# Kernel optimization log

Hardware: AMD Instinct MI355X
Metric: run time of the kernel (lower is better)

## Reference

```python
import jax, jax.numpy as jnp
import numpy as np

DIM = 512
HEADS = 8
D_HEAD = 64
INNER = HEADS * D_HEAD  # 512
CTX_DIM = 768
FF_INNER = 4 * DIM  # 2048
SCALE = D_HEAD ** -0.5
LN_EPS = 1e-5


def layer_norm(x, g, b):
    mu = jnp.mean(x, axis=-1, keepdims=True)
    var = jnp.var(x, axis=-1, keepdims=True)
    return (x - mu) * jax.lax.rsqrt(var + LN_EPS) * g + b


def attention(x, ctx, qw, kw, vw, ow, ob):
    B, N, _ = x.shape
    M = ctx.shape[1]
    q = (x @ qw).reshape(B, N, HEADS, D_HEAD).transpose(0, 2, 1, 3)
    k = (ctx @ kw).reshape(B, M, HEADS, D_HEAD).transpose(0, 2, 1, 3)
    v = (ctx @ vw).reshape(B, M, HEADS, D_HEAD).transpose(0, 2, 1, 3)
    sim = jnp.einsum('bhid,bhjd->bhij', q, k) * SCALE  # [B,H,N,M]
    attn = jax.nn.softmax(sim, axis=-1)
    out = jnp.einsum('bhij,bhjd->bhid', attn, v)
    out = out.transpose(0, 2, 1, 3).reshape(B, N, INNER)
    return out @ ow + ob


def setup_inputs() -> dict:
    key = jax.random.key(0)
    ks = jax.random.split(key, 20)
    r = lambda k, shp, s=0.02: jax.random.normal(k, shp, dtype=jnp.float32) * s
    return {
        'x': jax.random.normal(ks[0], (2, 4096, DIM), dtype=jnp.float32),
        'context': jax.random.normal(ks[1], (2, 256, CTX_DIM), dtype=jnp.float32),
        'q1_w': r(ks[2], (DIM, INNER)), 'k1_w': r(ks[3], (DIM, INNER)),
        'v1_w': r(ks[4], (DIM, INNER)), 'o1_w': r(ks[5], (INNER, DIM)),
        'o1_b': jnp.zeros((DIM,), jnp.float32),
        'q2_w': r(ks[6], (DIM, INNER)), 'k2_w': r(ks[7], (CTX_DIM, INNER)),
        'v2_w': r(ks[8], (CTX_DIM, INNER)), 'o2_w': r(ks[9], (INNER, DIM)),
        'o2_b': jnp.zeros((DIM,), jnp.float32),
        'ff_in_w': r(ks[10], (DIM, 2 * FF_INNER)), 'ff_in_b': jnp.zeros((2 * FF_INNER,), jnp.float32),
        'ff_out_w': r(ks[11], (FF_INNER, DIM)), 'ff_out_b': jnp.zeros((DIM,), jnp.float32),
        'ln1_g': jnp.ones((DIM,), jnp.float32), 'ln1_b': jnp.zeros((DIM,), jnp.float32),
        'ln2_g': jnp.ones((DIM,), jnp.float32), 'ln2_b': jnp.zeros((DIM,), jnp.float32),
        'ln3_g': jnp.ones((DIM,), jnp.float32), 'ln3_b': jnp.zeros((DIM,), jnp.float32),
    }


def reference(x, context, q1_w, k1_w, v1_w, o1_w, o1_b,
              q2_w, k2_w, v2_w, o2_w, o2_b,
              ff_in_w, ff_in_b, ff_out_w, ff_out_b,
              ln1_g, ln1_b, ln2_g, ln2_b, ln3_g, ln3_b):
    # self-attention + residual
    h = layer_norm(x, ln1_g, ln1_b)
    x = attention(h, h, q1_w, k1_w, v1_w, o1_w, o1_b) + x
    # cross-attention + residual
    h = layer_norm(x, ln2_g, ln2_b)
    x = attention(h, context, q2_w, k2_w, v2_w, o2_w, o2_b) + x
    # GEGLU feed-forward + residual (torch F.gelu is exact erf form)
    h = layer_norm(x, ln3_g, ln3_b)
    proj = h @ ff_in_w + ff_in_b
    val, gate = jnp.split(proj, 2, axis=-1)
    ff = (val * jax.nn.gelu(gate, approximate=False)) @ ff_out_w + ff_out_b
    return ff + x
```

## Files before the change

kernel.cpp:

```cpp
#include <hip/hip_runtime.h>
#include <hip/hip_bf16.h>
#include <cstdint>


typedef __bf16 bf16_t;
typedef __bf16 bf16x8 __attribute__((ext_vector_type(8)));
typedef float f32x4 __attribute__((ext_vector_type(4)));
typedef float f32x16 __attribute__((ext_vector_type(16)));

__device__ __forceinline__ bf16_t f2bf(float f) { return (bf16_t)f; }

__device__ __forceinline__ f32x4 mfma16(bf16x8 a, bf16x8 b, f32x4 c) {
  return __builtin_amdgcn_mfma_f32_16x16x32_bf16(a, b, c, 0, 0, 0);
}
__device__ __forceinline__ f32x16 mfma32(bf16x8 a, bf16x8 b, f32x16 c) {
  return __builtin_amdgcn_mfma_f32_32x32x16_bf16(a, b, c, 0, 0, 0);
}

__device__ __forceinline__ float gelu_exact(float x) {
  return 0.5f * x * (1.0f + erff(x * 0.70710678118654752f));
}

__device__ __forceinline__ void gload_lds16(const bf16_t* g, bf16_t* lds) {
  __builtin_amdgcn_global_load_lds(
      (const __attribute__((address_space(1))) unsigned int*)g,
      (__attribute__((address_space(3))) unsigned int*)lds, 16, 0, 0);
}

template <typename T>
__global__ __launch_bounds__(256) void ln_kernel(const T* __restrict__ in,
                                                 const float* __restrict__ gw,
                                                 const float* __restrict__ bw,
                                                 bf16_t* __restrict__ out) {
  int w = threadIdx.x >> 6, l = threadIdx.x & 63;
  size_t row = (size_t)blockIdx.x * 4 + w;
  float xs[8];
  if constexpr (sizeof(T) == 4) {
    const float* p = (const float*)in + row * 512 + l * 8;
    f32x4 va = *(const f32x4*)p;
    f32x4 vb = *(const f32x4*)(p + 4);
#pragma unroll
    for (int j = 0; j < 4; j++) { xs[j] = va[j]; xs[4 + j] = vb[j]; }
  } else {
    const bf16_t* p = (const bf16_t*)in + row * 512 + l * 8;
    bf16x8 v = *(const bf16x8*)p;
#pragma unroll
    for (int j = 0; j < 8; j++) xs[j] = (float)v[j];
  }
  float s = 0.f;
#pragma unroll
  for (int j = 0; j < 8; j++) s += xs[j];
#pragma unroll
  for (int m = 1; m < 64; m <<= 1) s += __shfl_xor(s, m);
  float mu = s * (1.0f / 512.0f);
  float v = 0.f;
#pragma unroll
  for (int j = 0; j < 8; j++) { float d = xs[j] - mu; v += d * d; }
#pragma unroll
  for (int m = 1; m < 64; m <<= 1) v += __shfl_xor(v, m);
  float rstd = rsqrtf(v * (1.0f / 512.0f) + 1e-5f);
  f32x4 g0 = *(const f32x4*)(gw + l * 8);
  f32x4 g1 = *(const f32x4*)(gw + l * 8 + 4);
  f32x4 b0 = *(const f32x4*)(bw + l * 8);
  f32x4 b1 = *(const f32x4*)(bw + l * 8 + 4);
  bf16x8 o;
#pragma unroll
  for (int j = 0; j < 4; j++) o[j] = f2bf((xs[j] - mu) * rstd * g0[j] + b0[j]);
#pragma unroll
  for (int j = 0; j < 4; j++) o[4 + j] = f2bf((xs[4 + j] - mu) * rstd * g1[j] + b1[j]);
  *(bf16x8*)(out + row * 512 + l * 8) = o;
}

struct WJob {
  const float* W;
  bf16_t* Wt;
  int K;
  int N;
  float sc;
  int tile0;
};
struct WJobs {
  WJob j[10];
};

__global__ __launch_bounds__(256) void wtrans_all_kernel(WJobs jobs) {
  __shared__ float t[32][33];
  int bid = blockIdx.x;
  int i = 0;
#pragma unroll
  for (int q = 1; q < 10; q++)
    if (bid >= jobs.j[q].tile0) i = q;
  WJob jb = jobs.j[i];
  int tt = bid - jb.tile0;
  int ktiles = jb.K >> 5;
  int k0 = (tt % ktiles) * 32, n0 = (tt / ktiles) * 32;
#pragma unroll
  for (int s = 0; s < 4; s++) {
    int idx = threadIdx.x + s * 256;
    int kk = idx >> 5, nn = idx & 31;
    t[kk][nn] = jb.W[(size_t)(k0 + kk) * jb.N + n0 + nn];
  }
  __syncthreads();
#pragma unroll
  for (int s = 0; s < 4; s++) {
    int idx = threadIdx.x + s * 256;
    int nn = idx >> 5, kk = idx & 31;
    jb.Wt[(size_t)(n0 + nn) * jb.K + k0 + kk] = f2bf(t[kk][nn] * jb.sc);
  }
}

__global__ __launch_bounds__(256) void cvt_kernel(const float* __restrict__ in,
                                                  bf16_t* __restrict__ out) {
  int i = (blockIdx.x * 256 + threadIdx.x) * 4;
  f32x4 v = *(const f32x4*)(in + i);
  out[i + 0] = f2bf(v[0]);
  out[i + 1] = f2bf(v[1]);
  out[i + 2] = f2bf(v[2]);
  out[i + 3] = f2bf(v[3]);
}

template <int BM, int BN, int EPI>
__global__ __launch_bounds__(256) void gemm_kernel(
    const bf16_t* __restrict__ A, const bf16_t* __restrict__ Bt,
    const float* __restrict__ bias, const void* __restrict__ res,
    void* __restrict__ outp, int M, int N, int K, int gateOff, int ldo) {
  constexpr int WR = BM / 2;
  constexpr int WN = BN / 2;
  constexpr int MF = WR / 16;
  constexpr int NF = WN / 16;
  constexpr int ABLK = BM / 64;
  constexpr int BROWS = (EPI == 2) ? 2 * BN : BN;
  constexpr int BBLK = BROWS / 64;
  __shared__ bf16_t Al[2][2][BM][32];
  __shared__ bf16_t Bl[2][2][BROWS][32];

  int tid = threadIdx.x;
  int w = tid >> 6, l = tid & 63;
  int wr = w >> 1, wc = w & 1;
  int lg = l >> 4, lc = l & 15;

  int ntiles = gridDim.y;
  int lin = blockIdx.y * gridDim.x + blockIdx.x;
  int cpx = (gridDim.x * gridDim.y) >> 3;
  int v = (lin & 7) * cpx + (lin >> 3);
  int m0 = (v / ntiles) * BM, n0 = (v % ntiles) * BN;

  f32x4 acc[MF][NF] = {};
  f32x4 acc2[MF][NF] = {};

  int srow = tid >> 2, scol = (tid & 3) * 8;
  const bf16_t* aP[ABLK];
#pragma unroll
  for (int i = 0; i < ABLK; i++)
    aP[i] = A + (size_t)(m0 + i * 64 + srow) * K + scol;
  const bf16_t* bP[BBLK];
  if (EPI == 2) {
    bP[0] = Bt + (size_t)(n0 + srow) * K + scol;
    bP[1] = Bt + (size_t)(n0 + gateOff + srow) * K + scol;
  } else {
#pragma unroll
    for (int i = 0; i < BBLK; i++)
      bP[i] = Bt + (size_t)(n0 + i * 64 + srow) * K + scol;
  }

  auto STAGE = [&](int buf, int k0) {
#pragma unroll
    for (int kh = 0; kh < 2; kh++) {
#pragma unroll
      for (int i = 0; i < ABLK; i++)
        gload_lds16(aP[i] + k0 + kh * 32, &Al[buf][kh][i * 64 + w * 16][0]);
#pragma unroll
      for (int i = 0; i < BBLK; i++)
        gload_lds16(bP[i] + k0 + kh * 32, &Bl[buf][kh][i * 64 + w * 16][0]);
    }
  };

  int nk = K / 64;
  int cur = 0;
  STAGE(0, 0);
  __syncthreads();

  for (int t = 0; t < nk; ++t) {
    if (t + 1 < nk) STAGE(cur ^ 1, (t + 1) * 64);

#pragma unroll
    for (int kh = 0; kh < 2; kh++) {
      bf16x8 af[MF];
#pragma unroll
      for (int mi = 0; mi < MF; mi++)
        af[mi] = *(const bf16x8*)&Al[cur][kh][wr * WR + mi * 16 + lc][lg * 8];
      bf16x8 bfr[NF];
#pragma unroll
      for (int ni = 0; ni < NF; ni++)
        bfr[ni] = *(const bf16x8*)&Bl[cur][kh][wc * WN + ni * 16 + lc][lg * 8];
#pragma unroll
      for (int mi = 0; mi < MF; mi++)
#pragma unroll
        for (int ni = 0; ni < NF; ni++)
          acc[mi][ni] = mfma16(af[mi], bfr[ni], acc[mi][ni]);
      if (EPI == 2) {
        bf16x8 bg[NF];
#pragma unroll
        for (int ni = 0; ni < NF; ni++)
          bg[ni] =
              *(const bf16x8*)&Bl[cur][kh][BN + wc * WN + ni * 16 + lc][lg * 8];
#pragma unroll
        for (int mi = 0; mi < MF; mi++)
#pragma unroll
          for (int ni = 0; ni < NF; ni++)
            acc2[mi][ni] = mfma16(af[mi], bg[ni], acc2[mi][ni]);
      }
    }
    __syncthreads();
    cur ^= 1;
  }

#pragma unroll
  for (int mi = 0; mi < MF; mi++) {
#pragma unroll
    for (int ni = 0; ni < NF; ni++) {
#pragma unroll
      for (int r = 0; r < 4; r++) {
        int row = m0 + wr * WR + mi * 16 + lg * 4 + r;
        int col = n0 + wc * WN + ni * 16 + lc;
        size_t idx = (size_t)row * ldo + col;
        float v2 = acc[mi][ni][r];
        if (EPI == 0) {
          ((bf16_t*)outp)[idx] = f2bf(v2);
        } else if (EPI == 3) {
          int cs = (col & ~15) | (lc & 3) | ((lc & 4) << 1) | ((lc & 8) >> 1);
          ((bf16_t*)outp)[(size_t)row * ldo + cs] = f2bf(v2);
        } else if (EPI == 4) {
          ((bf16_t*)outp)[idx] =
              f2bf(v2 + bias[col] + ((const float*)res)[idx]);
        } else if (EPI == 5) {
          ((bf16_t*)outp)[idx] =
              f2bf(v2 + bias[col] + (float)((const bf16_t*)res)[idx]);
        } else if (EPI == 6) {
          ((float*)outp)[idx] =
              v2 + bias[col] + (float)((const bf16_t*)res)[idx];
        } else {
          float g = acc2[mi][ni][r] + bias[col + gateOff];
          float val = v2 + bias[col];
          ((bf16_t*)outp)[idx] = f2bf(val * gelu_exact(g));
        }
      }
    }
  }
}

__global__ __launch_bounds__(256) void cross_fused_kernel(
    const bf16_t* __restrict__ hb, const bf16_t* __restrict__ q2t,
    bf16_t* __restrict__ qkb, const bf16_t* __restrict__ ctxb,
    const bf16_t* __restrict__ k2t, bf16_t* __restrict__ kb,
    const bf16_t* __restrict__ v2t, bf16_t* __restrict__ vtg2) {
  constexpr int BM = 64, BN = 128;
  constexpr int WR = 32, WN = 64, MF = 2, NF = 4;
  __shared__ bf16_t Al[2][2][BM][32];
  __shared__ bf16_t Bl[2][2][BN][32];

  const bf16_t* A;
  const bf16_t* Bt;
  bf16_t* outp;
  int K, m0;
  bool perm = false;
  if (blockIdx.z == 0) {
    A = hb; Bt = q2t; outp = qkb; K = 512; m0 = blockIdx.x * BM;
  } else {
    int bx = blockIdx.x;
    if (bx >= 16) return;
    K = 768;
    if (bx < 8) {
      A = ctxb; Bt = k2t; outp = kb; m0 = bx * BM;
    } else {
      A = v2t; Bt = ctxb; outp = vtg2; perm = true; m0 = (bx - 8) * BM;
    }
  }
  const int ldo = 512;
  int n0 = blockIdx.y * BN;

  int tid = threadIdx.x;
  int w = tid >> 6, l = tid & 63;
  int wr = w >> 1, wc = w & 1;
  int lg = l >> 4, lc = l & 15;

  f32x4 acc[MF][NF] = {};

  int srow = tid >> 2, scol = (tid & 3) * 8;
  const bf16_t* aP0 = A + (size_t)(m0 + srow) * K + scol;
  const bf16_t* bP0 = Bt + (size_t)(n0 + srow) * K + scol;
  const bf16_t* bP1 = Bt + (size_t)(n0 + 64 + srow) * K + scol;

  auto STAGE = [&](int buf, int k0) {
#pragma unroll
    for (int kh = 0; kh < 2; kh++) {
      gload_lds16(aP0 + k0 + kh * 32, &Al[buf][kh][w * 16][0]);
      gload_lds16(bP0 + k0 + kh * 32, &Bl[buf][kh][w * 16][0]);
      gload_lds16(bP1 + k0 + kh * 32, &Bl[buf][kh][64 + w * 16][0]);
    }
  };

  int nk = K / 64;
  int cur = 0;
  STAGE(0, 0);
  __syncthreads();

  for (int t = 0; t < nk; ++t) {
    if (t + 1 < nk) STAGE(cur ^ 1, (t + 1) * 64);
#pragma unroll
    for (int kh = 0; kh < 2; kh++) {
      bf16x8 af[MF];
#pragma unroll
      for (int mi = 0; mi < MF; mi++)
        af[mi] = *(const bf16x8*)&Al[cur][kh][wr * WR + mi * 16 + lc][lg * 8];
      bf16x8 bfr[NF];
#pragma unroll
      for (int ni = 0; ni < NF; ni++)
        bfr[ni] = *(const bf16x8*)&Bl[cur][kh][wc * WN + ni * 16 + lc][lg * 8];
#pragma unroll
      for (int mi = 0; mi < MF; mi++)
#pragma unroll
        for (int ni = 0; ni < NF; ni++)
          acc[mi][ni] = mfma16(af[mi], bfr[ni], acc[mi][ni]);
    }
    __syncthreads();
    cur ^= 1;
  }

#pragma unroll
  for (int mi = 0; mi < MF; mi++) {
#pragma unroll
    for (int ni = 0; ni < NF; ni++) {
#pragma unroll
      for (int r = 0; r < 4; r++) {
        int row = m0 + wr * WR + mi * 16 + lg * 4 + r;
        int col = n0 + wc * WN + ni * 16 + lc;
        int cs = perm ? ((col & ~15) | (lc & 3) | ((lc & 4) << 1) |
                         ((lc & 8) >> 1))
                      : col;
        outp[(size_t)row * ldo + cs] = f2bf(acc[mi][ni][r]);
      }
    }
  }
}

__global__ __launch_bounds__(256) void attn_kernel(
    const bf16_t* __restrict__ Q, int ldq, const bf16_t* __restrict__ Kb,
    int ldk, const bf16_t* __restrict__ Vt, bf16_t* __restrict__ O, int Mkv) {
  __shared__ bf16_t Klds[2][64][72];
  __shared__ bf16_t Vlds[2][64][72];

  int lin = blockIdx.x;
  int xcd = lin & 7, slot = lin >> 3;
  int pair = 2 * xcd + (slot >> 5);
  int qt = slot & 31;
  int head = pair & 7, b = pair >> 3;

  int tid = threadIdx.x;
  int w = tid >> 6, l = tid & 63;
  int ql = l & 31, hi = l >> 5;
  int ldv = 2 * Mkv;

  size_t qrow = (size_t)b * 4096 + qt * 128 + w * 32 + ql;
  const bf16_t* qp = Q + qrow * ldq + head * 64 + hi * 8;
  bf16x8 qf[4];
#pragma unroll
  for (int dk = 0; dk < 4; dk++) qf[dk] = *(const bf16x8*)(qp + dk * 16);

  f32x16 o0 = {}, o1 = {};
  f32x16 zacc = {};
  float mrun = -1e30f;

  bf16x8 vones;
#pragma unroll
  for (int j = 0; j < 8; j++) vones[j] = f2bf(1.0f);

  int key0 = tid >> 2, dc0 = (tid & 3) * 16;
  const bf16_t* kp = Kb + ((size_t)b * Mkv + key0) * ldk + head * 64 + dc0;
  const bf16_t* vp = Vt + (size_t)(head * 64 + key0) * ldv + b * Mkv + dc0;

  int nt = Mkv / 64;

  bf16x8 kc0 = *(const bf16x8*)kp, kc1 = *(const bf16x8*)(kp + 8);
  bf16x8 vc0 = *(const bf16x8*)vp, vc1 = *(const bf16x8*)(vp + 8);
  *(bf16x8*)&Klds[0][key0][dc0] = kc0;
  *(bf16x8*)&Klds[0][key0][dc0 + 8] = kc1;
  *(bf16x8*)&Vlds[0][key0][dc0] = vc0;
  *(bf16x8*)&Vlds[0][key0][dc0 + 8] = vc1;
  if (nt > 1) {
    kp += (size_t)64 * ldk;
    vp += 64;
    kc0 = *(const bf16x8*)kp;
    kc1 = *(const bf16x8*)(kp + 8);
    vc0 = *(const bf16x8*)vp;
    vc1 = *(const bf16x8*)(vp + 8);
  }
  __syncthreads();

  for (int t = 0; t < nt; ++t) {
    int cur = t & 1;

    f32x16 s0 = {}, s1 = {};
#pragma unroll
    for (int dk = 0; dk < 4; dk++) {
      bf16x8 a0 = *(const bf16x8*)&Klds[cur][ql][dk * 16 + hi * 8];
      bf16x8 a1 = *(const bf16x8*)&Klds[cur][32 + ql][dk * 16 + hi * 8];
      s0 = mfma32(a0, qf[dk], s0);
      s1 = mfma32(a1, qf[dk], s1);
    }

    float tmax = s0[0];
#pragma unroll
    for (int r = 1; r < 16; r++) tmax = fmaxf(tmax, s0[r]);
#pragma unroll
    for (int r = 0; r < 16; r++) tmax = fmaxf(tmax, s1[r]);
    tmax = fmaxf(tmax, __shfl_xor(tmax, 32));

    if (!__all(tmax <= mrun + 8.0f)) {
      float mnew = fmaxf(mrun, tmax);
      float resc = __builtin_amdgcn_exp2f(mrun - mnew);
      mrun = mnew;
#pragma unroll
      for (int r = 0; r < 16; r++) {
        float f = __shfl(resc, (r & 3) + 8 * (r >> 2) + 4 * hi);
        o0[r] *= f;
        o1[r] *= f;
        zacc[r] *= f;
      }
    }

    bf16x8 pa[4];
#pragma unroll
    for (int m = 0; m < 4; m++) {
#pragma unroll
      for (int j = 0; j < 8; j++) {
        float sv = (m < 2) ? s0[(m & 1) * 8 + j] : s1[(m & 1) * 8 + j];
        pa[m][j] = f2bf(__builtin_amdgcn_exp2f(sv - mrun));
      }
    }

#pragma unroll
    for (int m = 0; m < 4; m++) {
      zacc = mfma32(pa[m], vones, zacc);
      bf16x8 vb0 = *(const bf16x8*)&Vlds[cur][ql][m * 16 + hi * 8];
      bf16x8 vb1 = *(const bf16x8*)&Vlds[cur][32 + ql][m * 16 + hi * 8];
      o0 = mfma32(pa[m], vb0, o0);
      o1 = mfma32(pa[m], vb1, o1);
    }

    if (t + 1 < nt) {
      *(bf16x8*)&Klds[cur ^ 1][key0][dc0] = kc0;
      *(bf16x8*)&Klds[cur ^ 1][key0][dc0 + 8] = kc1;
      *(bf16x8*)&Vlds[cur ^ 1][key0][dc0] = vc0;
      *(bf16x8*)&Vlds[cur ^ 1][key0][dc0 + 8] = vc1;
      if (t + 2 < nt) {
        kp += (size_t)64 * ldk;
        vp += 64;
        kc0 = *(const bf16x8*)kp;
        kc1 = *(const bf16x8*)(kp + 8);
        vc0 = *(const bf16x8*)vp;
        vc1 = *(const bf16x8*)(vp + 8);
      }
      __syncthreads();
    }
  }

  size_t ob = ((size_t)b * 4096 + qt * 128 + w * 32) * 512 + head * 64;
#pragma unroll
  for (int r = 0; r < 16; r++) {
    float inv = 1.0f / zacc[r];
    int q = (r & 3) + 8 * (r >> 2) + 4 * hi;
    O[ob + (size_t)q * 512 + ql] = f2bf(o0[r] * inv);
    O[ob + (size_t)q * 512 + 32 + ql] = f2bf(o1[r] * inv);
  }
}

extern "C" void kernel_launch(void* const* d_in, const int* in_sizes, int n_in,
                              void* d_out, int out_size, void* d_ws,
                              size_t ws_size, hipStream_t stream) {
  const float* x = (const float*)d_in[0];
  const float* ctx = (const float*)d_in[1];
  const float* q1_w = (const float*)d_in[2];
  const float* k1_w = (const float*)d_in[3];
  const float* v1_w = (const float*)d_in[4];
  const float* o1_w = (const float*)d_in[5];
  const float* o1_b = (const float*)d_in[6];
  const float* q2_w = (const float*)d_in[7];
  const float* k2_w = (const float*)d_in[8];
  const float* v2_w = (const float*)d_in[9];
  const float* o2_w = (const float*)d_in[10];
  const float* o2_b = (const float*)d_in[11];
  const float* ff_in_w = (const float*)d_in[12];
  const float* ff_in_b = (const float*)d_in[13];
  const float* ff_out_w = (const float*)d_in[14];
  const float* ff_out_b = (const float*)d_in[15];
  const float* ln1_g = (const float*)d_in[16];
  const float* ln1_b = (const float*)d_in[17];
  const float* ln2_g = (const float*)d_in[18];
  const float* ln2_b = (const float*)d_in[19];
  const float* ln3_g = (const float*)d_in[20];
  const float* ln3_b = (const float*)d_in[21];

  char* ws = (char*)d_ws;
  bf16_t* xrb1 = (bf16_t*)(ws + 0);
  bf16_t* xrb2 = (bf16_t*)(ws + 8388608);
  bf16_t* hb = (bf16_t*)(ws + 16777216);
  bf16_t* qkb = (bf16_t*)(ws + 25165824);
  bf16_t* ao = (bf16_t*)(ws + 41943040);
  bf16_t* ffmid = qkb;
  bf16_t* kb = (bf16_t*)(ws + 50331648);
  bf16_t* vtg2 = (bf16_t*)(ws + 50855936);
  bf16_t* ctxb = (bf16_t*)(ws + 51380224);
  bf16_t* wts = (bf16_t*)(ws + 58720256);
  bf16_t* vtg = (bf16_t*)(ws + 69730304);

  bf16_t* q1t = wts + 0;
  bf16_t* k1t = wts + 262144;
  bf16_t* v1t = wts + 524288;
  bf16_t* o1t = wts + 786432;
  bf16_t* q2t = wts + 1048576;
  bf16_t* k2t = wts + 1310720;
  bf16_t* v2t = wts + 1703936;
  bf16_t* o2t = wts + 2097152;
  bf16_t* ffint = wts + 2359296;
  bf16_t* ffoutt = wts + 4456448;

  const float QS = 0.125f * 1.44269504f;

  WJobs jobs;
  auto setj = [&](int i, const float* W, bf16_t* Wt, int K, int N, float sc,
                  int tile0) {
    jobs.j[i] = WJob{W, Wt, K, N, sc, tile0};
  };
  setj(0, q1_w, q1t, 512, 512, QS, 0);
  setj(1, k1_w, k1t, 512, 512, 1.0f, 256);
  setj(2, v1_w, v1t, 512, 512, 1.0f, 512);
  setj(3, o1_w, o1t, 512, 512, 1.0f, 768);
  setj(4, q2_w, q2t, 512, 512, QS, 1024);
  setj(5, k2_w, k2t, 768, 512, 1.0f, 1280);
  setj(6, v2_w, v2t, 768, 512, 1.0f, 1664);
  setj(7, o2_w, o2t, 512, 512, 1.0f, 2048);
  setj(8, ff_in_w, ffint, 512, 4096, 1.0f, 2304);
  setj(9, ff_out_w, ffoutt, 2048, 512, 1.0f, 4352);
  wtrans_all_kernel<<<5376, 256, 0, stream>>>(jobs);
  cvt_kernel<<<384, 256, 0, stream>>>(ctx, ctxb);

  ln_kernel<float><<<2048, 256, 0, stream>>>(x, ln1_g, ln1_b, hb);
  gemm_kernel<128, 128, 0><<<dim3(64, 8), 256, 0, stream>>>(
      hb, q1t, nullptr, nullptr, qkb, 8192, 1024, 512, 0, 1024);
  gemm_kernel<64, 128, 3><<<dim3(8, 64), 256, 0, stream>>>(
      v1t, hb, nullptr, nullptr, vtg, 512, 8192, 512, 0, 8192);
  attn_kernel<<<512, 256, 0, stream>>>(qkb, 1024, qkb + 512, 1024, vtg, ao,
                                       4096);
  gemm_kernel<64, 64, 4><<<dim3(128, 8), 256, 0, stream>>>(
      ao, o1t, o1_b, x, xrb1, 8192, 512, 512, 0, 512);

  ln_kernel<bf16_t><<<2048, 256, 0, stream>>>(xrb1, ln2_g, ln2_b, hb);
  cross_fused_kernel<<<dim3(128, 4, 2), 256, 0, stream>>>(
      hb, q2t, qkb, ctxb, k2t, kb, v2t, vtg2);
  attn_kernel<<<512, 256, 0, stream>>>(qkb, 512, kb, 512, vtg2, ao, 256);
  gemm_kernel<64, 64, 5><<<dim3(128, 8), 256, 0, stream>>>(
      ao, o2t, o2_b, xrb1, xrb2, 8192, 512, 512, 0, 512);

  ln_kernel<bf16_t><<<2048, 256, 0, stream>>>(xrb2, ln3_g, ln3_b, hb);
  gemm_kernel<128, 64, 2><<<dim3(64, 32), 256, 0, stream>>>(
      hb, ffint, ff_in_b, nullptr, ffmid, 8192, 2048, 512, 2048, 2048);
  gemm_kernel<64, 128, 6><<<dim3(128, 4), 256, 0, stream>>>(
      ffmid, ffoutt, ff_out_b, xrb2, (float*)d_out, 8192, 512, 2048, 0, 512);
}
```

Baseline: 279.8 us.

## Split self-attention KV range across two blocks and merge with combine kernel

```diff
diff --git a/kernel.cpp b/kernel.cpp
--- a/kernel.cpp
+++ b/kernel.cpp
@@ -5,6 +5,7 @@
 
 typedef __bf16 bf16_t;
 typedef __bf16 bf16x8 __attribute__((ext_vector_type(8)));
+typedef __bf16 bf16x4 __attribute__((ext_vector_type(4)));
 typedef float f32x4 __attribute__((ext_vector_type(4)));
 typedef float f32x16 __attribute__((ext_vector_type(16)));
 
@@ -344,17 +345,26 @@
   }
 }
 
+template <bool SPLIT>
 __global__ __launch_bounds__(256) void attn_kernel(
     const bf16_t* __restrict__ Q, int ldq, const bf16_t* __restrict__ Kb,
-    int ldk, const bf16_t* __restrict__ Vt, bf16_t* __restrict__ O, int Mkv) {
+    int ldk, const bf16_t* __restrict__ Vt, bf16_t* __restrict__ O, int Mkv,
+    bf16_t* __restrict__ po, float* __restrict__ pm, float* __restrict__ pz) {
   __shared__ bf16_t Klds[2][64][72];
   __shared__ bf16_t Vlds[2][64][72];
 
   int lin = blockIdx.x;
   int xcd = lin & 7, slot = lin >> 3;
-  int pair = 2 * xcd + (slot >> 5);
-  int qt = slot & 31;
+  int chunk = 0, rest = slot;
+  if (SPLIT) {
+    chunk = slot >> 6;
+    rest = slot & 63;
+  }
+  int pair = 2 * xcd + (rest >> 5);
+  int qt = rest & 31;
   int head = pair & 7, b = pair >> 3;
+  int kvlen = SPLIT ? (Mkv >> 1) : Mkv;
+  int kv0 = chunk * kvlen;
 
   int tid = threadIdx.x;
   int w = tid >> 6, l = tid & 63;
@@ -376,10 +386,12 @@
   for (int j = 0; j < 8; j++) vones[j] = f2bf(1.0f);
 
   int key0 = tid >> 2, dc0 = (tid & 3) * 16;
-  const bf16_t* kp = Kb + ((size_t)b * Mkv + key0) * ldk + head * 64 + dc0;
-  const bf16_t* vp = Vt + (size_t)(head * 64 + key0) * ldv + b * Mkv + dc0;
-
-  int nt = Mkv / 64;
+  const bf16_t* kp =
+      Kb + ((size_t)b * Mkv + kv0 + key0) * ldk + head * 64 + dc0;
+  const bf16_t* vp =
+      Vt + (size_t)(head * 64 + key0) * ldv + b * Mkv + kv0 + dc0;
+
+  int nt = kvlen / 64;
 
   bf16x8 kc0 = *(const bf16x8*)kp, kc1 = *(const bf16x8*)(kp + 8);
   bf16x8 vc0 = *(const bf16x8*)vp, vc1 = *(const bf16x8*)(vp + 8);
@@ -401,6 +413,7 @@
     int cur = t & 1;
 
     f32x16 s0 = {}, s1 = {};
+    __builtin_amdgcn_s_setprio(1);
 #pragma unroll
     for (int dk = 0; dk < 4; dk++) {
       bf16x8 a0 = *(const bf16x8*)&Klds[cur][ql][dk * 16 + hi * 8];
@@ -408,6 +421,7 @@
       s0 = mfma32(a0, qf[dk], s0);
       s1 = mfma32(a1, qf[dk], s1);
     }
+    __builtin_amdgcn_s_setprio(0);
 
     float tmax = s0[0];
 #pragma unroll
@@ -439,6 +453,7 @@
       }
     }
 
+    __builtin_amdgcn_s_setprio(1);
 #pragma unroll
     for (int m = 0; m < 4; m++) {
       zacc = mfma32(pa[m], vones, zacc);
@@ -447,6 +462,7 @@
       o0 = mfma32(pa[m], vb0, o0);
       o1 = mfma32(pa[m], vb1, o1);
     }
+    __builtin_amdgcn_s_setprio(0);
 
     if (t + 1 < nt) {
       *(bf16x8*)&Klds[cur ^ 1][key0][dc0] = kc0;
@@ -465,14 +481,48 @@
     }
   }
 
-  size_t ob = ((size_t)b * 4096 + qt * 128 + w * 32) * 512 + head * 64;
-#pragma unroll
-  for (int r = 0; r < 16; r++) {
-    float inv = 1.0f / zacc[r];
-    int q = (r & 3) + 8 * (r >> 2) + 4 * hi;
-    O[ob + (size_t)q * 512 + ql] = f2bf(o0[r] * inv);
-    O[ob + (size_t)q * 512 + 32 + ql] = f2bf(o1[r] * inv);
-  }
+  if (SPLIT) {
+    size_t qbase = ((size_t)(b * 8 + head)) * 4096 + qt * 128 + w * 32;
+#pragma unroll
+    for (int r = 0; r < 16; r++) {
+      int q = (r & 3) + 8 * (r >> 2) + 4 * hi;
+      size_t fq = (size_t)chunk * 65536 + qbase + q;
+      po[fq * 64 + ql] = f2bf(o0[r]);
+      po[fq * 64 + 32 + ql] = f2bf(o1[r]);
+      if (ql == 0) pz[fq] = zacc[r];
+    }
+    if (hi == 0) pm[(size_t)chunk * 65536 + qbase + ql] = mrun;
+  } else {
+    size_t ob = ((size_t)b * 4096 + qt * 128 + w * 32) * 512 + head * 64;
+#pragma unroll
+    for (int r = 0; r < 16; r++) {
+      float inv = 1.0f / zacc[r];
+      int q = (r & 3) + 8 * (r >> 2) + 4 * hi;
+      O[ob + (size_t)q * 512 + ql] = f2bf(o0[r] * inv);
+      O[ob + (size_t)q * 512 + 32 + ql] = f2bf(o1[r] * inv);
+    }
+  }
+}
+
+__global__ __launch_bounds__(256) void attn_combine_kernel(
+    const bf16_t* __restrict__ po, const float* __restrict__ pm,
+    const float* __restrict__ pz, bf16_t* __restrict__ O) {
+  int idx = blockIdx.x * 256 + threadIdx.x;
+  int fq = idx >> 4, d0 = (idx & 15) * 4;
+  float m1 = pm[fq], m2 = pm[65536 + fq];
+  float z1 = pz[fq], z2 = pz[65536 + fq];
+  float M = fmaxf(m1, m2);
+  float w1 = __builtin_amdgcn_exp2f(m1 - M);
+  float w2 = __builtin_amdgcn_exp2f(m2 - M);
+  float inv = 1.0f / (z1 * w1 + z2 * w2);
+  bf16x4 a = *(const bf16x4*)&po[(size_t)fq * 64 + d0];
+  bf16x4 c = *(const bf16x4*)&po[((size_t)65536 + fq) * 64 + d0];
+  int b = fq >> 15, head = (fq >> 12) & 7, tok = fq & 4095;
+  bf16x4 out;
+#pragma unroll
+  for (int j = 0; j < 4; j++)
+    out[j] = f2bf(((float)a[j] * w1 + (float)c[j] * w2) * inv);
+  *(bf16x4*)(O + ((size_t)(b * 4096 + tok)) * 512 + head * 64 + d0) = out;
 }
 
 extern "C" void kernel_launch(void* const* d_in, const int* in_sizes, int n_in,
@@ -504,6 +554,7 @@
   char* ws = (char*)d_ws;
   bf16_t* xrb1 = (bf16_t*)(ws + 0);
   bf16_t* xrb2 = (bf16_t*)(ws + 8388608);
+  bf16_t* po = (bf16_t*)(ws + 0);
   bf16_t* hb = (bf16_t*)(ws + 16777216);
   bf16_t* qkb = (bf16_t*)(ws + 25165824);
   bf16_t* ao = (bf16_t*)(ws + 41943040);
@@ -511,6 +562,8 @@
   bf16_t* kb = (bf16_t*)(ws + 50331648);
   bf16_t* vtg2 = (bf16_t*)(ws + 50855936);
   bf16_t* ctxb = (bf16_t*)(ws + 51380224);
+  float* pm = (float*)(ws + 52166656);
+  float* pz = (float*)(ws + 52690944);
   bf16_t* wts = (bf16_t*)(ws + 58720256);
   bf16_t* vtg = (bf16_t*)(ws + 69730304);
 
@@ -550,15 +603,17 @@
       hb, q1t, nullptr, nullptr, qkb, 8192, 1024, 512, 0, 1024);
   gemm_kernel<64, 128, 3><<<dim3(8, 64), 256, 0, stream>>>(
       v1t, hb, nullptr, nullptr, vtg, 512, 8192, 512, 0, 8192);
-  attn_kernel<<<512, 256, 0, stream>>>(qkb, 1024, qkb + 512, 1024, vtg, ao,
-                                       4096);
+  attn_kernel<true><<<1024, 256, 0, stream>>>(qkb, 1024, qkb + 512, 1024, vtg,
+                                              nullptr, 4096, po, pm, pz);
+  attn_combine_kernel<<<4096, 256, 0, stream>>>(po, pm, pz, ao);
   gemm_kernel<64, 64, 4><<<dim3(128, 8), 256, 0, stream>>>(
       ao, o1t, o1_b, x, xrb1, 8192, 512, 512, 0, 512);
 
   ln_kernel<bf16_t><<<2048, 256, 0, stream>>>(xrb1, ln2_g, ln2_b, hb);
   cross_fused_kernel<<<dim3(128, 4, 2), 256, 0, stream>>>(
       hb, q2t, qkb, ctxb, k2t, kb, v2t, vtg2);
-  attn_kernel<<<512, 256, 0, stream>>>(qkb, 512, kb, 512, vtg2, ao, 256);
+  attn_kernel<false><<<512, 256, 0, stream>>>(qkb, 512, kb, 512, vtg2, ao, 256,
+                                              nullptr, nullptr, nullptr);
   gemm_kernel<64, 64, 5><<<dim3(128, 8), 256, 0, stream>>>(
       ao, o2t, o2_b, xrb1, xrb2, 8192, 512, 512, 0, 512);
 
```

Result: slower. 287.0 us (+2.5%).
